# Performance work log

Hardware: AMD Instinct MI355X
Metric: run time of the kernel (lower is better)

Reference implementation:

```python
import jax, jax.numpy as jnp
import numpy as np

E, I, O = 8, 1024, 1024   # num_experts, in_features, out_features
B = 16                    # number of molecular systems (segments)
N = 16384                 # total rows (atoms * coeffs); sum(mole_sizes) == N


def setup_inputs() -> dict:
    key = jax.random.key(0)
    k1, k2, k3, k4 = jax.random.split(key, 4)
    scale = (1.0 / I) ** 0.5
    x = jax.random.normal(k1, (N, I), dtype=jnp.float32)
    # init_linear: uniform(-k, k) with k = sqrt(1/in_features)
    weights = scale * 2.0 * (jax.random.uniform(k2, (E, O, I), dtype=jnp.float32) - 0.5)
    bias = scale * 2.0 * (jax.random.uniform(k3, (O,), dtype=jnp.float32) - 0.5)
    expert_mixing_coefficients = jax.random.uniform(k4, (B, E), dtype=jnp.float32)
    # segment sizes per system; equal sizes summing exactly to N (static under jit)
    mole_sizes = jnp.full((B,), N // B, dtype=jnp.int32)
    return {
        "x": x,
        "weights": weights,
        "bias": bias,
        "expert_mixing_coefficients": expert_mixing_coefficients,
        "mole_sizes": mole_sizes,
    }


def reference(x, weights, bias, expert_mixing_coefficients, mole_sizes):
    # Original: W_b = einsum('eoi,be->bio', weights, coeff); then segment_mm
    # applies x_seg_b @ W_b for each row-segment b.  By linearity this equals
    # projecting x through each expert and mixing with per-row coefficients,
    # which avoids materializing [B, I, O] synthesized weights per segment
    # while computing identical math.
    n = x.shape[0]
    b = expert_mixing_coefficients.shape[0]
    seg_id = jnp.repeat(jnp.arange(b), mole_sizes, total_repeat_length=n)  # [N]
    ct = expert_mixing_coefficients[seg_id]                               # [N, E]
    proj = jnp.einsum('ni,eoi->neo', x, weights)                          # [N, E, O]
    y = jnp.einsum('neo,ne->no', proj, ct) + bias                         # [N, O]
    return y
```

## Files before the change

kernel.cpp:

```cpp
#include <hip/hip_runtime.h>
#include <hip/hip_bf16.h>
#include <stdint.h>

constexpr int E_NUM  = 8;
constexpr int I_DIM  = 1024;
constexpr int O_DIM  = 1024;
constexpr int B_SEG  = 16;
constexpr int N_ROWS = 16384;

constexpr int BM = 128, BN = 128, BK = 32;

typedef __bf16 bf16x8 __attribute__((ext_vector_type(8)));
typedef float  f32x4  __attribute__((ext_vector_type(4)));
typedef unsigned short ushortx8 __attribute__((ext_vector_type(8)));

__device__ __forceinline__ unsigned short f2bf(float f) {
    unsigned int u = __float_as_uint(f);
    u += 0x7fffu + ((u >> 16) & 1u);
    return (unsigned short)(u >> 16);
}

__global__ __launch_bounds__(256) void cvt_x(const float* __restrict__ x,
                                             unsigned short* __restrict__ xb) {
    size_t idx = ((size_t)blockIdx.x * 256 + threadIdx.x) * 16;
    const float4* p = (const float4*)(x + idx);
    float4 v0 = p[0], v1 = p[1], v2 = p[2], v3 = p[3];
    ushortx8 o0, o1;
    o0[0] = f2bf(v0.x); o0[1] = f2bf(v0.y); o0[2] = f2bf(v0.z); o0[3] = f2bf(v0.w);
    o0[4] = f2bf(v1.x); o0[5] = f2bf(v1.y); o0[6] = f2bf(v1.z); o0[7] = f2bf(v1.w);
    o1[0] = f2bf(v2.x); o1[1] = f2bf(v2.y); o1[2] = f2bf(v2.z); o1[3] = f2bf(v2.w);
    o1[4] = f2bf(v3.x); o1[5] = f2bf(v3.y); o1[6] = f2bf(v3.z); o1[7] = f2bf(v3.w);
    *(ushortx8*)(xb + idx)     = o0;
    *(ushortx8*)(xb + idx + 8) = o1;
}

__global__ __launch_bounds__(256) void synth_w(const float* __restrict__ w,
                                               const float* __restrict__ coeff,
                                               unsigned short* __restrict__ wb) {
    __shared__ float sc[B_SEG * E_NUM];
    int tid = threadIdx.x;
    if (tid < B_SEG * E_NUM) sc[tid] = coeff[tid];
    __syncthreads();

    size_t idx = ((size_t)blockIdx.x * 256 + tid) * 8;
    float4 wv0[E_NUM], wv1[E_NUM];
#pragma unroll
    for (int e = 0; e < E_NUM; e++) {
        const float4* p = (const float4*)(w + (size_t)e * O_DIM * I_DIM + idx);
        wv0[e] = p[0];
        wv1[e] = p[1];
    }

#pragma unroll
    for (int b = 0; b < B_SEG; b++) {
        float a[8] = {0,0,0,0,0,0,0,0};
#pragma unroll
        for (int e = 0; e < E_NUM; e++) {
            float c = sc[b * E_NUM + e];
            a[0] += c * wv0[e].x; a[1] += c * wv0[e].y;
            a[2] += c * wv0[e].z; a[3] += c * wv0[e].w;
            a[4] += c * wv1[e].x; a[5] += c * wv1[e].y;
            a[6] += c * wv1[e].z; a[7] += c * wv1[e].w;
        }
        ushortx8 o;
#pragma unroll
        for (int j = 0; j < 8; j++) o[j] = f2bf(a[j]);
        *(ushortx8*)(wb + (size_t)b * O_DIM * I_DIM + idx) = o;
    }
}

__global__ __launch_bounds__(256) void gemm_moe(
    const unsigned short* __restrict__ xb,
    const unsigned short* __restrict__ wb,
    const float* __restrict__ bias,
    const int* __restrict__ msz,
    float* __restrict__ out)
{
    __shared__ __align__(16) unsigned short sA[BM * BK];
    __shared__ __align__(16) unsigned short sB[BN * BK];

    const int lid  = blockIdx.x;
    const int xcd  = lid & 7;
    const int idx  = lid >> 3;
    const int seg  = (xcd << 1) | (idx >> 6);
    const int s    = idx & 63;
    const int mloc = s >> 3;
    const int nblk = s & 7;

    int off = 0;
    for (int b = 0; b < seg; b++) off += msz[b];
    const int row0 = off + mloc * BM;
    const int col0 = nblk * BN;
    const unsigned short* wseg = wb + (size_t)seg * O_DIM * I_DIM;

    const int tid  = threadIdx.x;
    const int wave = tid >> 6;
    const int lane = tid & 63;
    const int wm = wave >> 1, wn = wave & 1;
    const int quad = lane >> 4, l16 = lane & 15;

    const int srow   = wave * 32 + (lane >> 2);
    const int schunk = (lane & 3) ^ ((lane >> 3) & 3);
    const int scol   = schunk * 8;

    const unsigned short* gA = xb   + (size_t)(row0 + srow) * I_DIM + scol;
    const unsigned short* gB = wseg + (size_t)(col0 + srow) * I_DIM + scol;
    const int ldsOfs0 = (wave * 32) * BK;
    const int ldsOfs1 = (wave * 32 + 16) * BK;

    const int rchunk = (quad ^ ((l16 >> 1) & 3)) * 8;

    f32x4 acc[4][4];
#pragma unroll
    for (int m = 0; m < 4; m++)
#pragma unroll
        for (int n = 0; n < 4; n++)
            acc[m][n] = (f32x4){0.f, 0.f, 0.f, 0.f};

#pragma unroll 1
    for (int k0 = 0; k0 < I_DIM; k0 += BK) {
        __builtin_amdgcn_global_load_lds(
            (const __attribute__((address_space(1))) void*)(gA + k0),
            (__attribute__((address_space(3))) void*)(&sA[ldsOfs0]), 16, 0, 0);
        __builtin_amdgcn_global_load_lds(
            (const __attribute__((address_space(1))) void*)(gA + 16 * I_DIM + k0),
            (__attribute__((address_space(3))) void*)(&sA[ldsOfs1]), 16, 0, 0);
        __builtin_amdgcn_global_load_lds(
            (const __attribute__((address_space(1))) void*)(gB + k0),
            (__attribute__((address_space(3))) void*)(&sB[ldsOfs0]), 16, 0, 0);
        __builtin_amdgcn_global_load_lds(
            (const __attribute__((address_space(1))) void*)(gB + 16 * I_DIM + k0),
            (__attribute__((address_space(3))) void*)(&sB[ldsOfs1]), 16, 0, 0);
        __syncthreads();

        bf16x8 af[4], bfr[4];
#pragma unroll
        for (int m = 0; m < 4; m++)
            af[m] = *(const bf16x8*)&sA[(wm * 64 + m * 16 + l16) * BK + rchunk];
#pragma unroll
        for (int n = 0; n < 4; n++)
            bfr[n] = *(const bf16x8*)&sB[(wn * 64 + n * 16 + l16) * BK + rchunk];

#pragma unroll
        for (int m = 0; m < 4; m++)
#pragma unroll
            for (int n = 0; n < 4; n++)
                acc[m][n] = __builtin_amdgcn_mfma_f32_16x16x32_bf16(
                    af[m], bfr[n], acc[m][n], 0, 0, 0);

        __syncthreads();
    }

    float bv[4];
#pragma unroll
    for (int n = 0; n < 4; n++)
        bv[n] = bias[col0 + wn * 64 + n * 16 + l16];

#pragma unroll
    for (int m = 0; m < 4; m++) {
#pragma unroll
        for (int r = 0; r < 4; r++) {
            int row = row0 + wm * 64 + m * 16 + quad * 4 + r;
            float* po = out + (size_t)row * O_DIM + col0 + wn * 64 + l16;
#pragma unroll
            for (int n = 0; n < 4; n++)
                po[n * 16] = acc[m][n][r] + bv[n];
        }
    }
}

extern "C" void kernel_launch(void* const* d_in, const int* in_sizes, int n_in,
                              void* d_out, int out_size, void* d_ws, size_t ws_size,
                              hipStream_t stream) {
    const float* x     = (const float*)d_in[0];
    const float* w     = (const float*)d_in[1];
    const float* bias  = (const float*)d_in[2];
    const float* coeff = (const float*)d_in[3];
    const int*   msz   = (const int*)d_in[4];
    float* out = (float*)d_out;

    unsigned short* xb = (unsigned short*)d_ws;
    unsigned short* wb = xb + (size_t)N_ROWS * I_DIM;

    int cvt_blocks   = (int)(((size_t)N_ROWS * I_DIM) / (256 * 16));
    int synth_blocks = (int)(((size_t)O_DIM * I_DIM) / (256 * 8));

    cvt_x<<<cvt_blocks, 256, 0, stream>>>(x, xb);
    synth_w<<<synth_blocks, 256, 0, stream>>>(w, coeff, wb);

    gemm_moe<<<1024, 256, 0, stream>>>(xb, wb, bias, msz, out);
}
```

Before: 208.2 us.

## Enlarge GEMM tiles to 256x256x64 with double-buffered LDS and 512 threads

The GEMM tile grows from 128x128x32 to 256x256x64, with 8 waves per block each holding an 8x4 MFMA accumulator set. LDS is double-buffered so global-to-LDS loads for tile k+2 overlap MFMA work on the current tile, and LDS reads use inline ds_read_b128 with an XOR swizzle. It also adds s_setprio around the MFMA bursts. The grid shrinks to 256 blocks, so on a GPU with many CUs, occupancy and tail balance may suffer, and register pressure rises.

```diff
diff --git a/kernel.cpp b/kernel.cpp
--- a/kernel.cpp
+++ b/kernel.cpp
@@ -8,7 +8,8 @@
 constexpr int B_SEG  = 16;
 constexpr int N_ROWS = 16384;
 
-constexpr int BM = 128, BN = 128, BK = 32;
+constexpr int BM = 256, BN = 256, BK = 64;
+constexpr int NT = I_DIM / BK;
 
 typedef __bf16 bf16x8 __attribute__((ext_vector_type(8)));
 typedef float  f32x4  __attribute__((ext_vector_type(4)));
@@ -69,101 +70,151 @@
     }
 }
 
-__global__ __launch_bounds__(256) void gemm_moe(
+__device__ __forceinline__ bf16x8 lds_read_b128(unsigned addr) {
+    bf16x8 r;
+    asm volatile("ds_read_b128 %0, %1" : "=v"(r) : "v"(addr));
+    return r;
+}
+
+__global__ __launch_bounds__(512, 2) void gemm_moe(
     const unsigned short* __restrict__ xb,
     const unsigned short* __restrict__ wb,
     const float* __restrict__ bias,
     const int* __restrict__ msz,
     float* __restrict__ out)
 {
-    __shared__ __align__(16) unsigned short sA[BM * BK];
-    __shared__ __align__(16) unsigned short sB[BN * BK];
+    __shared__ __align__(16) unsigned short sA[2][BM * BK];
+    __shared__ __align__(16) unsigned short sB[2][BN * BK];
 
     const int lid  = blockIdx.x;
     const int xcd  = lid & 7;
     const int idx  = lid >> 3;
-    const int seg  = (xcd << 1) | (idx >> 6);
-    const int s    = idx & 63;
-    const int mloc = s >> 3;
-    const int nblk = s & 7;
+    const int seg  = (xcd << 1) | (idx >> 4);
+    const int t    = idx & 15;
+    const int mblk = t >> 2;
+    const int nblk = t & 3;
 
     int off = 0;
     for (int b = 0; b < seg; b++) off += msz[b];
-    const int row0 = off + mloc * BM;
+    const int row0 = off + mblk * BM;
     const int col0 = nblk * BN;
     const unsigned short* wseg = wb + (size_t)seg * O_DIM * I_DIM;
 
     const int tid  = threadIdx.x;
     const int wave = tid >> 6;
     const int lane = tid & 63;
-    const int wm = wave >> 1, wn = wave & 1;
+    const int wr = wave >> 2, wc = wave & 3;
     const int quad = lane >> 4, l16 = lane & 15;
 
-    const int srow   = wave * 32 + (lane >> 2);
-    const int schunk = (lane & 3) ^ ((lane >> 3) & 3);
-    const int scol   = schunk * 8;
-
-    const unsigned short* gA = xb   + (size_t)(row0 + srow) * I_DIM + scol;
-    const unsigned short* gB = wseg + (size_t)(col0 + srow) * I_DIM + scol;
-    const int ldsOfs0 = (wave * 32) * BK;
-    const int ldsOfs1 = (wave * 32 + 16) * BK;
-
-    const int rchunk = (quad ^ ((l16 >> 1) & 3)) * 8;
-
-    f32x4 acc[4][4];
-#pragma unroll
-    for (int m = 0; m < 4; m++)
-#pragma unroll
-        for (int n = 0; n < 4; n++)
+    const int srow   = lane >> 3;
+    const int schunk = (lane & 7) ^ srow;
+    const unsigned short* gA = xb   + (size_t)(row0 + wave * 32 + srow) * I_DIM + schunk * 8;
+    const unsigned short* gB = wseg + (size_t)(col0 + wave * 32 + srow) * I_DIM + schunk * 8;
+
+    const unsigned ldsA0 = (unsigned)(size_t)((__attribute__((address_space(3))) unsigned short*)&sA[0][0]);
+    const unsigned ldsB0 = (unsigned)(size_t)((__attribute__((address_space(3))) unsigned short*)&sB[0][0]);
+    constexpr unsigned BUFB = (unsigned)(BM * BK * 2);
+    const unsigned rp0 = (unsigned)(((quad    ) ^ (l16 & 7)) * 16);
+    const unsigned rp1 = (unsigned)(((quad + 4) ^ (l16 & 7)) * 16);
+    const unsigned rowA = (unsigned)((wr * 128 + l16) * 128);
+    const unsigned rowB = (unsigned)((wc * 64  + l16) * 128);
+    const unsigned rdA0 = ldsA0 + rowA + rp0, rdA1 = ldsA0 + rowA + rp1;
+    const unsigned rdB0 = ldsB0 + rowB + rp0, rdB1 = ldsB0 + rowB + rp1;
+
+#define STAGE_TILE(CUR, K0)                                                            \
+    do {                                                                               \
+        _Pragma("unroll")                                                              \
+        for (int j_ = 0; j_ < 4; ++j_) {                                               \
+            __builtin_amdgcn_global_load_lds(                                          \
+                (const __attribute__((address_space(1))) void*)(gA + (K0) + j_ * 8 * I_DIM), \
+                (__attribute__((address_space(3))) void*)(&sA[(CUR)][(wave * 32 + j_ * 8) * BK]), \
+                16, 0, 0);                                                             \
+            __builtin_amdgcn_global_load_lds(                                          \
+                (const __attribute__((address_space(1))) void*)(gB + (K0) + j_ * 8 * I_DIM), \
+                (__attribute__((address_space(3))) void*)(&sB[(CUR)][(wave * 32 + j_ * 8) * BK]), \
+                16, 0, 0);                                                             \
+        }                                                                              \
+    } while (0)
+
+    f32x4 acc[8][4];
+#pragma unroll
+    for (int m = 0; m < 8; ++m)
+#pragma unroll
+        for (int n = 0; n < 4; ++n)
             acc[m][n] = (f32x4){0.f, 0.f, 0.f, 0.f};
 
-#pragma unroll 1
-    for (int k0 = 0; k0 < I_DIM; k0 += BK) {
-        __builtin_amdgcn_global_load_lds(
-            (const __attribute__((address_space(1))) void*)(gA + k0),
-            (__attribute__((address_space(3))) void*)(&sA[ldsOfs0]), 16, 0, 0);
-        __builtin_amdgcn_global_load_lds(
-            (const __attribute__((address_space(1))) void*)(gA + 16 * I_DIM + k0),
-            (__attribute__((address_space(3))) void*)(&sA[ldsOfs1]), 16, 0, 0);
-        __builtin_amdgcn_global_load_lds(
-            (const __attribute__((address_space(1))) void*)(gB + k0),
-            (__attribute__((address_space(3))) void*)(&sB[ldsOfs0]), 16, 0, 0);
-        __builtin_amdgcn_global_load_lds(
-            (const __attribute__((address_space(1))) void*)(gB + 16 * I_DIM + k0),
-            (__attribute__((address_space(3))) void*)(&sB[ldsOfs1]), 16, 0, 0);
-        __syncthreads();
-
-        bf16x8 af[4], bfr[4];
-#pragma unroll
-        for (int m = 0; m < 4; m++)
-            af[m] = *(const bf16x8*)&sA[(wm * 64 + m * 16 + l16) * BK + rchunk];
-#pragma unroll
-        for (int n = 0; n < 4; n++)
-            bfr[n] = *(const bf16x8*)&sB[(wn * 64 + n * 16 + l16) * BK + rchunk];
-
-#pragma unroll
-        for (int m = 0; m < 4; m++)
-#pragma unroll
-            for (int n = 0; n < 4; n++)
+    STAGE_TILE(0, 0);
+    STAGE_TILE(1, BK);
+    asm volatile("s_waitcnt vmcnt(8)");
+    __builtin_amdgcn_sched_barrier(0);
+    __builtin_amdgcn_s_barrier();
+
+#pragma unroll 2
+    for (int kt = 0; kt < NT; ++kt) {
+        const int cur = kt & 1;
+        const unsigned bo = (unsigned)cur * BUFB;
+
+        bf16x8 af[8], bfr[4];
+
+#pragma unroll
+        for (int m = 0; m < 8; ++m) af[m] = lds_read_b128(rdA0 + bo + m * 2048);
+#pragma unroll
+        for (int n = 0; n < 4; ++n) bfr[n] = lds_read_b128(rdB0 + bo + n * 2048);
+        asm volatile("s_waitcnt lgkmcnt(0)");
+        __builtin_amdgcn_sched_barrier(0);
+        __builtin_amdgcn_s_setprio(1);
+#pragma unroll
+        for (int m = 0; m < 8; ++m)
+#pragma unroll
+            for (int n = 0; n < 4; ++n)
                 acc[m][n] = __builtin_amdgcn_mfma_f32_16x16x32_bf16(
                     af[m], bfr[n], acc[m][n], 0, 0, 0);
-
-        __syncthreads();
-    }
+        __builtin_amdgcn_s_setprio(0);
+        __builtin_amdgcn_sched_barrier(0);
+
+#pragma unroll
+        for (int m = 0; m < 8; ++m) af[m] = lds_read_b128(rdA1 + bo + m * 2048);
+#pragma unroll
+        for (int n = 0; n < 4; ++n) bfr[n] = lds_read_b128(rdB1 + bo + n * 2048);
+        asm volatile("s_waitcnt lgkmcnt(0)");
+        __builtin_amdgcn_sched_barrier(0);
+        __builtin_amdgcn_s_setprio(1);
+#pragma unroll
+        for (int m = 0; m < 8; ++m)
+#pragma unroll
+            for (int n = 0; n < 4; ++n)
+                acc[m][n] = __builtin_amdgcn_mfma_f32_16x16x32_bf16(
+                    af[m], bfr[n], acc[m][n], 0, 0, 0);
+        __builtin_amdgcn_s_setprio(0);
+        __builtin_amdgcn_sched_barrier(0);
+
+        if (kt < NT - 1) {
+            __builtin_amdgcn_s_barrier();
+            if (kt < NT - 2) {
+                STAGE_TILE(cur, (kt + 2) * BK);
+                asm volatile("s_waitcnt vmcnt(8)");
+            } else {
+                asm volatile("s_waitcnt vmcnt(0)");
+            }
+            __builtin_amdgcn_sched_barrier(0);
+            __builtin_amdgcn_s_barrier();
+        }
+    }
+#undef STAGE_TILE
 
     float bv[4];
 #pragma unroll
-    for (int n = 0; n < 4; n++)
-        bv[n] = bias[col0 + wn * 64 + n * 16 + l16];
-
-#pragma unroll
-    for (int m = 0; m < 4; m++) {
-#pragma unroll
-        for (int r = 0; r < 4; r++) {
-            int row = row0 + wm * 64 + m * 16 + quad * 4 + r;
-            float* po = out + (size_t)row * O_DIM + col0 + wn * 64 + l16;
-#pragma unroll
-            for (int n = 0; n < 4; n++)
+    for (int n = 0; n < 4; ++n)
+        bv[n] = bias[col0 + wc * 64 + n * 16 + l16];
+
+#pragma unroll
+    for (int m = 0; m < 8; ++m) {
+#pragma unroll
+        for (int r = 0; r < 4; ++r) {
+            int row = row0 + wr * 128 + m * 16 + quad * 4 + r;
+            float* po = out + (size_t)row * O_DIM + col0 + wc * 64 + l16;
+#pragma unroll
+            for (int n = 0; n < 4; ++n)
                 po[n * 16] = acc[m][n][r] + bv[n];
         }
     }
@@ -188,5 +239,5 @@
     cvt_x<<<cvt_blocks, 256, 0, stream>>>(x, xb);
     synth_w<<<synth_blocks, 256, 0, stream>>>(w, coeff, wb);
 
-    gemm_moe<<<1024, 256, 0, stream>>>(xb, wb, bias, msz, out);
-}
+    gemm_moe<<<B_SEG * (1024 / BM) * (1024 / BN), 512, 0, stream>>>(xb, wb, bias, msz, out);
+}
```

After: 191.3 us. 8.1% less time.

## Pipeline GEMM with 256x256 tiles, multi-stage LDS ring and fused prep kernel

Applied to the files above, without the earlier changes.

The two preprocessing kernels are merged into one launch that splits blocks between x conversion and weight synthesis. The GEMM moves to 256x256x64 tiles with 8 waves and a 128KB LDS ring buffer. Global-to-LDS staging of future k-tiles is interleaved with four MFMA phases per tile, using explicit barriers, waitcnt and setprio to overlap memory with compute. This aims to raise arithmetic intensity and hide load latency. The cost is heavy LDS use that limits occupancy, and fragile hand-written synchronisation.

```diff
diff --git a/kernel.cpp b/kernel.cpp
--- a/kernel.cpp
+++ b/kernel.cpp
@@ -8,11 +8,15 @@
 constexpr int B_SEG  = 16;
 constexpr int N_ROWS = 16384;
 
-constexpr int BM = 128, BN = 128, BK = 32;
+constexpr int BM = 256, BN = 256, BK = 64;
+constexpr int NT = I_DIM / BK;
 
 typedef __bf16 bf16x8 __attribute__((ext_vector_type(8)));
 typedef float  f32x4  __attribute__((ext_vector_type(4)));
 typedef unsigned short ushortx8 __attribute__((ext_vector_type(8)));
+
+#define AS1 __attribute__((address_space(1)))
+#define AS3 __attribute__((address_space(3)))
 
 __device__ __forceinline__ unsigned short f2bf(float f) {
     unsigned int u = __float_as_uint(f);
@@ -20,151 +24,209 @@
     return (unsigned short)(u >> 16);
 }
 
-__global__ __launch_bounds__(256) void cvt_x(const float* __restrict__ x,
-                                             unsigned short* __restrict__ xb) {
-    size_t idx = ((size_t)blockIdx.x * 256 + threadIdx.x) * 16;
-    const float4* p = (const float4*)(x + idx);
-    float4 v0 = p[0], v1 = p[1], v2 = p[2], v3 = p[3];
-    ushortx8 o0, o1;
-    o0[0] = f2bf(v0.x); o0[1] = f2bf(v0.y); o0[2] = f2bf(v0.z); o0[3] = f2bf(v0.w);
-    o0[4] = f2bf(v1.x); o0[5] = f2bf(v1.y); o0[6] = f2bf(v1.z); o0[7] = f2bf(v1.w);
-    o1[0] = f2bf(v2.x); o1[1] = f2bf(v2.y); o1[2] = f2bf(v2.z); o1[3] = f2bf(v2.w);
-    o1[4] = f2bf(v3.x); o1[5] = f2bf(v3.y); o1[6] = f2bf(v3.z); o1[7] = f2bf(v3.w);
-    *(ushortx8*)(xb + idx)     = o0;
-    *(ushortx8*)(xb + idx + 8) = o1;
-}
-
-__global__ __launch_bounds__(256) void synth_w(const float* __restrict__ w,
-                                               const float* __restrict__ coeff,
-                                               unsigned short* __restrict__ wb) {
+__global__ __launch_bounds__(256) void prep(const float* __restrict__ x,
+                                            unsigned short* __restrict__ xb,
+                                            const float* __restrict__ w,
+                                            const float* __restrict__ coeff,
+                                            unsigned short* __restrict__ wb) {
     __shared__ float sc[B_SEG * E_NUM];
-    int tid = threadIdx.x;
-    if (tid < B_SEG * E_NUM) sc[tid] = coeff[tid];
-    __syncthreads();
-
-    size_t idx = ((size_t)blockIdx.x * 256 + tid) * 8;
-    float4 wv0[E_NUM], wv1[E_NUM];
-#pragma unroll
-    for (int e = 0; e < E_NUM; e++) {
-        const float4* p = (const float4*)(w + (size_t)e * O_DIM * I_DIM + idx);
-        wv0[e] = p[0];
-        wv1[e] = p[1];
+    const int bid = blockIdx.x;
+    const int tid = threadIdx.x;
+
+    if (bid < 4096) {
+        size_t idx = ((size_t)bid * 256 + tid) * 16;
+        const float4* p = (const float4*)(x + idx);
+        float4 v0 = p[0], v1 = p[1], v2 = p[2], v3 = p[3];
+        ushortx8 o0, o1;
+        o0[0] = f2bf(v0.x); o0[1] = f2bf(v0.y); o0[2] = f2bf(v0.z); o0[3] = f2bf(v0.w);
+        o0[4] = f2bf(v1.x); o0[5] = f2bf(v1.y); o0[6] = f2bf(v1.z); o0[7] = f2bf(v1.w);
+        o1[0] = f2bf(v2.x); o1[1] = f2bf(v2.y); o1[2] = f2bf(v2.z); o1[3] = f2bf(v2.w);
+        o1[4] = f2bf(v3.x); o1[5] = f2bf(v3.y); o1[6] = f2bf(v3.z); o1[7] = f2bf(v3.w);
+        *(ushortx8*)(xb + idx)     = o0;
+        *(ushortx8*)(xb + idx + 8) = o1;
+    } else {
+        if (tid < B_SEG * E_NUM) sc[tid] = coeff[tid];
+        __syncthreads();
+
+        size_t idx = ((size_t)(bid - 4096) * 256 + tid) * 8;
+        float4 wv0[E_NUM], wv1[E_NUM];
+#pragma unroll
+        for (int e = 0; e < E_NUM; e++) {
+            const float4* p = (const float4*)(w + (size_t)e * O_DIM * I_DIM + idx);
+            wv0[e] = p[0];
+            wv1[e] = p[1];
+        }
+
+#pragma unroll
+        for (int b = 0; b < B_SEG; b++) {
+            float a[8] = {0,0,0,0,0,0,0,0};
+#pragma unroll
+            for (int e = 0; e < E_NUM; e++) {
+                float c = sc[b * E_NUM + e];
+                a[0] += c * wv0[e].x; a[1] += c * wv0[e].y;
+                a[2] += c * wv0[e].z; a[3] += c * wv0[e].w;
+                a[4] += c * wv1[e].x; a[5] += c * wv1[e].y;
+                a[6] += c * wv1[e].z; a[7] += c * wv1[e].w;
+            }
+            ushortx8 o;
+#pragma unroll
+            for (int j = 0; j < 8; j++) o[j] = f2bf(a[j]);
+            *(ushortx8*)(wb + (size_t)b * O_DIM * I_DIM + idx) = o;
+        }
     }
-
-#pragma unroll
-    for (int b = 0; b < B_SEG; b++) {
-        float a[8] = {0,0,0,0,0,0,0,0};
-#pragma unroll
-        for (int e = 0; e < E_NUM; e++) {
-            float c = sc[b * E_NUM + e];
-            a[0] += c * wv0[e].x; a[1] += c * wv0[e].y;
-            a[2] += c * wv0[e].z; a[3] += c * wv0[e].w;
-            a[4] += c * wv1[e].x; a[5] += c * wv1[e].y;
-            a[6] += c * wv1[e].z; a[7] += c * wv1[e].w;
-        }
-        ushortx8 o;
-#pragma unroll
-        for (int j = 0; j < 8; j++) o[j] = f2bf(a[j]);
-        *(ushortx8*)(wb + (size_t)b * O_DIM * I_DIM + idx) = o;
-    }
-}
-
-__global__ __launch_bounds__(256) void gemm_moe(
+}
+
+__device__ __forceinline__ bf16x8 lds_read_b128(unsigned addr) {
+    bf16x8 r;
+    asm volatile("ds_read_b128 %0, %1" : "=v"(r) : "v"(addr));
+    return r;
+}
+
+__global__ __launch_bounds__(512, 2) void gemm_moe(
     const unsigned short* __restrict__ xb,
     const unsigned short* __restrict__ wb,
     const float* __restrict__ bias,
     const int* __restrict__ msz,
     float* __restrict__ out)
 {
-    __shared__ __align__(16) unsigned short sA[BM * BK];
-    __shared__ __align__(16) unsigned short sB[BN * BK];
+    __shared__ __align__(16) char sLDS[131072];
 
     const int lid  = blockIdx.x;
     const int xcd  = lid & 7;
     const int idx  = lid >> 3;
-    const int seg  = (xcd << 1) | (idx >> 6);
-    const int s    = idx & 63;
-    const int mloc = s >> 3;
-    const int nblk = s & 7;
+    const int seg  = (xcd << 1) | (idx >> 4);
+    const int t16  = idx & 15;
+    const int mblk = t16 >> 2;
+    const int nblk = t16 & 3;
 
     int off = 0;
     for (int b = 0; b < seg; b++) off += msz[b];
-    const int row0 = off + mloc * BM;
+    const int row0 = off + mblk * BM;
     const int col0 = nblk * BN;
     const unsigned short* wseg = wb + (size_t)seg * O_DIM * I_DIM;
 
     const int tid  = threadIdx.x;
     const int wave = tid >> 6;
     const int lane = tid & 63;
-    const int wm = wave >> 1, wn = wave & 1;
+    const int wr = wave >> 2, wc = wave & 3;
     const int quad = lane >> 4, l16 = lane & 15;
 
-    const int srow   = wave * 32 + (lane >> 2);
-    const int schunk = (lane & 3) ^ ((lane >> 3) & 3);
-    const int scol   = schunk * 8;
-
-    const unsigned short* gA = xb   + (size_t)(row0 + srow) * I_DIM + scol;
-    const unsigned short* gB = wseg + (size_t)(col0 + srow) * I_DIM + scol;
-    const int ldsOfs0 = (wave * 32) * BK;
-    const int ldsOfs1 = (wave * 32 + 16) * BK;
-
-    const int rchunk = (quad ^ ((l16 >> 1) & 3)) * 8;
-
-    f32x4 acc[4][4];
-#pragma unroll
-    for (int m = 0; m < 4; m++)
-#pragma unroll
-        for (int n = 0; n < 4; n++)
+    const int srow8  = lane >> 3;
+    const int schunk = (lane & 7) ^ srow8;
+    const unsigned short* gA0 = xb   + (size_t)(row0 + wave * 8 + srow8) * I_DIM + schunk * 8;
+    const unsigned short* gA1 = gA0 + (size_t)128 * I_DIM;
+    const unsigned short* gB0 = wseg + (size_t)(col0 + wave * 8 + srow8) * I_DIM + schunk * 8;
+    const unsigned short* gB1 = gB0 + (size_t)128 * I_DIM;
+
+    const unsigned rdA0 = (unsigned)((wr * 16 + l16) * 128 + (((0 + quad) ^ (l16 & 7)) * 16));
+    const unsigned rdA1 = (unsigned)((wr * 16 + l16) * 128 + (((4 + quad) ^ (l16 & 7)) * 16));
+    const unsigned rdB0 = (unsigned)(65536 + (wc * 16 + l16) * 128 + (((0 + quad) ^ (l16 & 7)) * 16));
+    const unsigned rdB1 = (unsigned)(65536 + (wc * 16 + l16) * 128 + (((4 + quad) ^ (l16 & 7)) * 16));
+
+    bf16x8 af[4][2], bfr[2][2];
+    f32x4 acc[8][4];
+#pragma unroll
+    for (int m = 0; m < 8; ++m)
+#pragma unroll
+        for (int n = 0; n < 4; ++n)
             acc[m][n] = (f32x4){0.f, 0.f, 0.f, 0.f};
 
+#define LOAD_A(S) do { _Pragma("unroll") for (int mm = 0; mm < 4; ++mm) {           \
+        af[mm][0] = lds_read_b128(rdA0 + (S) * 16384u + mm * 4096u);                \
+        af[mm][1] = lds_read_b128(rdA1 + (S) * 16384u + mm * 4096u); } } while (0)
+#define LOAD_B(S) do { _Pragma("unroll") for (int nn = 0; nn < 2; ++nn) {           \
+        bfr[nn][0] = lds_read_b128(rdB0 + (S) * 16384u + nn * 8192u);               \
+        bfr[nn][1] = lds_read_b128(rdB1 + (S) * 16384u + nn * 8192u); } } while (0)
+
+#define STAGE_A(H, S, ST) do {                                                      \
+        const unsigned short* g_ = ((H) ? gA1 : gA0) + (size_t)(ST) * 64;           \
+        __builtin_amdgcn_global_load_lds((const AS1 void*)g_,                       \
+            (AS3 void*)(sLDS + (S) * 16384 + wave * 1024), 16, 0, 0);               \
+        __builtin_amdgcn_global_load_lds((const AS1 void*)(g_ + (size_t)64 * I_DIM),\
+            (AS3 void*)(sLDS + (S) * 16384 + 8192 + wave * 1024), 16, 0, 0); } while (0)
+#define STAGE_B(H, S, ST) do {                                                      \
+        const unsigned short* g_ = ((H) ? gB1 : gB0) + (size_t)(ST) * 64;           \
+        __builtin_amdgcn_global_load_lds((const AS1 void*)g_,                       \
+            (AS3 void*)(sLDS + 65536 + (S) * 16384 + wave * 1024), 16, 0, 0);       \
+        __builtin_amdgcn_global_load_lds((const AS1 void*)(g_ + (size_t)64 * I_DIM),\
+            (AS3 void*)(sLDS + 65536 + (S) * 16384 + 8192 + wave * 1024), 16, 0, 0); } while (0)
+
+#define MFMA_Q(MH, NH) do { _Pragma("unroll") for (int mm = 0; mm < 4; ++mm)        \
+        _Pragma("unroll") for (int nn = 0; nn < 2; ++nn)                            \
+        _Pragma("unroll") for (int kk = 0; kk < 2; ++kk)                            \
+            acc[(MH) * 4 + mm][(NH) * 2 + nn] =                                     \
+                __builtin_amdgcn_mfma_f32_16x16x32_bf16(af[mm][kk], bfr[nn][kk],    \
+                    acc[(MH) * 4 + mm][(NH) * 2 + nn], 0, 0, 0); } while (0)
+
+#define PH_MID() do { __builtin_amdgcn_s_barrier();                                 \
+        asm volatile("s_waitcnt lgkmcnt(0)");                                       \
+        __builtin_amdgcn_sched_barrier(0);                                          \
+        __builtin_amdgcn_s_setprio(1); } while (0)
+#define PH_END() do { __builtin_amdgcn_s_setprio(0);                                \
+        __builtin_amdgcn_sched_barrier(0);                                          \
+        __builtin_amdgcn_s_barrier(); } while (0)
+
+#define TILE(RS0, RS1, SS01, SS23, ST1, ST2) do {                                   \
+                                                                 \
+        LOAD_A(RS0); LOAD_B(RS1); STAGE_A(1, SS01, ST1);                            \
+        PH_MID(); MFMA_Q(0, 1); PH_END();                                           \
+                                                                 \
+        LOAD_B(RS0); STAGE_B(1, SS01, ST1);                                         \
+        PH_MID(); MFMA_Q(0, 0); PH_END();                                           \
+                                                 \
+        LOAD_A(RS1); STAGE_A(0, SS23, ST2);                                         \
+        PH_MID(); MFMA_Q(1, 0); PH_END();                                           \
+                                                                 \
+        LOAD_B(RS1); STAGE_B(0, SS23, ST2);                                         \
+        PH_MID(); MFMA_Q(1, 1);                                                     \
+        __builtin_amdgcn_s_setprio(0);                                              \
+        __builtin_amdgcn_sched_barrier(0);                                          \
+        asm volatile("s_waitcnt vmcnt(4)");                                         \
+        __builtin_amdgcn_sched_barrier(0);                                          \
+        __builtin_amdgcn_s_barrier();                                               \
+    } while (0)
+
+    STAGE_A(0, 0, 0); STAGE_B(0, 0, 0);
+    STAGE_A(1, 1, 0); STAGE_B(1, 1, 0);
+    STAGE_A(0, 2, 1); STAGE_B(0, 2, 1);
+    asm volatile("s_waitcnt vmcnt(4)");
+    __builtin_amdgcn_sched_barrier(0);
+    __builtin_amdgcn_s_barrier();
+
 #pragma unroll 1
-    for (int k0 = 0; k0 < I_DIM; k0 += BK) {
-        __builtin_amdgcn_global_load_lds(
-            (const __attribute__((address_space(1))) void*)(gA + k0),
-            (__attribute__((address_space(3))) void*)(&sA[ldsOfs0]), 16, 0, 0);
-        __builtin_amdgcn_global_load_lds(
-            (const __attribute__((address_space(1))) void*)(gA + 16 * I_DIM + k0),
-            (__attribute__((address_space(3))) void*)(&sA[ldsOfs1]), 16, 0, 0);
-        __builtin_amdgcn_global_load_lds(
-            (const __attribute__((address_space(1))) void*)(gB + k0),
-            (__attribute__((address_space(3))) void*)(&sB[ldsOfs0]), 16, 0, 0);
-        __builtin_amdgcn_global_load_lds(
-            (const __attribute__((address_space(1))) void*)(gB + 16 * I_DIM + k0),
-            (__attribute__((address_space(3))) void*)(&sB[ldsOfs1]), 16, 0, 0);
-        __syncthreads();
-
-        bf16x8 af[4], bfr[4];
-#pragma unroll
-        for (int m = 0; m < 4; m++)
-            af[m] = *(const bf16x8*)&sA[(wm * 64 + m * 16 + l16) * BK + rchunk];
-#pragma unroll
-        for (int n = 0; n < 4; n++)
-            bfr[n] = *(const bf16x8*)&sB[(wn * 64 + n * 16 + l16) * BK + rchunk];
-
-#pragma unroll
-        for (int m = 0; m < 4; m++)
-#pragma unroll
-            for (int n = 0; n < 4; n++)
-                acc[m][n] = __builtin_amdgcn_mfma_f32_16x16x32_bf16(
-                    af[m], bfr[n], acc[m][n], 0, 0, 0);
-
-        __syncthreads();
+    for (int tp = 0; tp < 8; ++tp) {
+        const int t0 = 2 * tp, t1 = t0 + 1;
+        const int s1a = (t0 + 1 < 15) ? t0 + 1 : 15;
+        const int s2a = (t0 + 2 < 15) ? t0 + 2 : 15;
+        const int s1b = (t1 + 1 < 15) ? t1 + 1 : 15;
+        const int s2b = (t1 + 2 < 15) ? t1 + 2 : 15;
+        TILE(0, 1, 3, 0, s1a, s2a);
+        TILE(2, 3, 1, 2, s1b, s2b);
     }
 
+#undef TILE
+#undef PH_END
+#undef PH_MID
+#undef MFMA_Q
+#undef STAGE_B
+#undef STAGE_A
+#undef LOAD_B
+#undef LOAD_A
+
     float bv[4];
 #pragma unroll
-    for (int n = 0; n < 4; n++)
-        bv[n] = bias[col0 + wn * 64 + n * 16 + l16];
-
-#pragma unroll
-    for (int m = 0; m < 4; m++) {
-#pragma unroll
-        for (int r = 0; r < 4; r++) {
-            int row = row0 + wm * 64 + m * 16 + quad * 4 + r;
-            float* po = out + (size_t)row * O_DIM + col0 + wn * 64 + l16;
-#pragma unroll
-            for (int n = 0; n < 4; n++)
-                po[n * 16] = acc[m][n][r] + bv[n];
+    for (int n = 0; n < 4; ++n)
+        bv[n] = bias[col0 + n * 64 + wc * 16 + l16];
+
+#pragma unroll
+    for (int m = 0; m < 8; ++m) {
+#pragma unroll
+        for (int r = 0; r < 4; ++r) {
+            int row = row0 + m * 32 + wr * 16 + quad * 4 + r;
+            float* po = out + (size_t)row * O_DIM + col0 + wc * 16 + l16;
+#pragma unroll
+            for (int n = 0; n < 4; ++n)
+                po[n * 64] = acc[m][n][r] + bv[n];
         }
     }
 }
@@ -182,11 +244,7 @@
     unsigned short* xb = (unsigned short*)d_ws;
     unsigned short* wb = xb + (size_t)N_ROWS * I_DIM;
 
-    int cvt_blocks   = (int)(((size_t)N_ROWS * I_DIM) / (256 * 16));
-    int synth_blocks = (int)(((size_t)O_DIM * I_DIM) / (256 * 8));
-
-    cvt_x<<<cvt_blocks, 256, 0, stream>>>(x, xb);
-    synth_w<<<synth_blocks, 256, 0, stream>>>(w, coeff, wb);
-
-    gemm_moe<<<1024, 256, 0, stream>>>(xb, wb, bias, msz, out);
-}
+    prep<<<4096 + 512, 256, 0, stream>>>(x, xb, w, coeff, wb);
+
+    gemm_moe<<<B_SEG * (1024 / BM) * (1024 / BN), 512, 0, stream>>>(xb, wb, bias, msz, out);
+}
```

New measurement: 197.0 us. 5.3% less time.
